# Kernel tuning notes

Hardware: AMD Instinct MI355X
Metric: run time of the kernel (lower is better)

Reference implementation:

```python
import jax, jax.numpy as jnp
import numpy as np

T = 4
THRESH = 1.0
TAU = 1.0
GAMA = 0.5

# Heaviside spike with Gaussian surrogate gradient (SgNormal)
@jax.custom_vjp
def sg_normal(x):
    return (x > 0).astype(x.dtype)

def _sg_fwd(x):
    return (x > 0).astype(x.dtype), x

def _sg_bwd(x, g):
    inv_norm = 1.0 / (GAMA * np.sqrt(2.0 * np.pi).astype(np.float32))
    return (g * jnp.exp(-(x * x) / (2.0 * GAMA * GAMA)) * inv_norm,)

sg_normal.defvjp(_sg_fwd, _sg_bwd)


def setup_inputs() -> dict:
    key = jax.random.key(0)
    x = jax.random.normal(key, (T, 64, 128, 32, 32), dtype=jnp.float32)
    return {"x": x}


def reference(x):
    # LIF recurrence over T timesteps: mem = mem*tau + x[t]; spike = H(mem - thresh); mem = (1-spike)*mem
    def step(mem, xt):
        mem = mem * TAU + xt
        spike = sg_normal(mem - THRESH)
        mem = (1.0 - spike) * mem
        return mem, spike

    mem0 = jnp.zeros(x.shape[1:], dtype=x.dtype)
    _, spikes = jax.lax.scan(step, mem0, x)  # spikes: [T, B, C, H, W]
    return spikes
```

## Files before the change

### kernel.cpp

```cpp
#include <hip/hip_runtime.h>


#define LIF_T 4
#define CHUNKS 4

typedef float f32x4 __attribute__((ext_vector_type(4)));

__device__ __forceinline__ f32x4 lif_step(f32x4& mem, f32x4 xt) {
    mem.x += xt.x;
    mem.y += xt.y;
    mem.z += xt.z;
    mem.w += xt.w;
    f32x4 sp;
    sp.x = (mem.x > 1.0f) ? 1.0f : 0.0f;
    sp.y = (mem.y > 1.0f) ? 1.0f : 0.0f;
    sp.z = (mem.z > 1.0f) ? 1.0f : 0.0f;
    sp.w = (mem.w > 1.0f) ? 1.0f : 0.0f;
    mem.x = (sp.x > 0.f) ? 0.f : mem.x;
    mem.y = (sp.y > 0.f) ? 0.f : mem.y;
    mem.z = (sp.z > 0.f) ? 0.f : mem.z;
    mem.w = (sp.w > 0.f) ? 0.f : mem.w;
    return sp;
}

__global__ __launch_bounds__(256) void
lif_spike_kernel(const float* __restrict__ x, float* __restrict__ out, int n_vec) {
    const int base = blockIdx.x * (256 * CHUNKS) + threadIdx.x;
    const f32x4* __restrict__ xv = reinterpret_cast<const f32x4*>(x);
    f32x4* __restrict__ ov = reinterpret_cast<f32x4*>(out);

    if (base + (CHUNKS - 1) * 256 < n_vec) {
        f32x4 mem[CHUNKS];
#pragma unroll
        for (int c = 0; c < CHUNKS; ++c) mem[c] = (f32x4){0.f, 0.f, 0.f, 0.f};

#pragma unroll
        for (int t = 0; t < LIF_T; ++t) {
            const size_t p = (size_t)t * n_vec + base;
            f32x4 xt[CHUNKS];
#pragma unroll
            for (int c = 0; c < CHUNKS; ++c) xt[c] = xv[p + c * 256];
#pragma unroll
            for (int c = 0; c < CHUNKS; ++c) {
                f32x4 sp = lif_step(mem[c], xt[c]);
                __builtin_nontemporal_store(sp, &ov[p + c * 256]);
            }
        }
    } else {
        f32x4 memc[CHUNKS];
#pragma unroll
        for (int c = 0; c < CHUNKS; ++c) memc[c] = (f32x4){0.f, 0.f, 0.f, 0.f};
#pragma unroll
        for (int t = 0; t < LIF_T; ++t) {
#pragma unroll
            for (int c = 0; c < CHUNKS; ++c) {
                int idx = base + c * 256;
                if (idx < n_vec) {
                    f32x4 sp = lif_step(memc[c], xv[(size_t)t * n_vec + idx]);
                    __builtin_nontemporal_store(sp, &ov[(size_t)t * n_vec + idx]);
                }
            }
        }
    }
}

extern "C" void kernel_launch(void* const* d_in, const int* in_sizes, int n_in,
                              void* d_out, int out_size, void* d_ws, size_t ws_size,
                              hipStream_t stream) {
    const float* x = (const float*)d_in[0];
    float* out = (float*)d_out;

    int n = out_size / LIF_T;
    int n_vec = n / 4;

    const int block = 256;
    int grid = (n_vec + block * CHUNKS - 1) / (block * CHUNKS);
    lif_spike_kernel<<<grid, block, 0, stream>>>(x, out, n_vec);
}
```

Baseline: 227.3 us.

## Stage LIF inputs through LDS with async global_load_lds and smaller per-block chunks

Every thread now issues all four timesteps' loads up front as direct global-to-LDS transfers (`global_load_lds`, 16 bytes per lane). It then waits on vmcnt before each timestep and reads its inputs from LDS. The aim is to have more memory requests in flight per thread before any compute starts, which should hide latency on this bandwidth-bound kernel. Per-block work drops from 1024 to 512 float4 per timestep, which doubles the grid. The trade-offs are LDS allocation, manual waitcnt accounting that stores also affect, and reliance on 16-byte LDS DMA support.

```diff
diff --git a/kernel.cpp b/kernel.cpp
--- a/kernel.cpp
+++ b/kernel.cpp
@@ -2,9 +2,12 @@
 
 
 #define LIF_T 4
-#define CHUNKS 4
+#define CHUNK_F4 512
 
 typedef float f32x4 __attribute__((ext_vector_type(4)));
+
+#define AS1 __attribute__((address_space(1)))
+#define AS3 __attribute__((address_space(3)))
 
 __device__ __forceinline__ f32x4 lif_step(f32x4& mem, f32x4 xt) {
     mem.x += xt.x;
@@ -25,36 +28,53 @@
 
 __global__ __launch_bounds__(256) void
 lif_spike_kernel(const float* __restrict__ x, float* __restrict__ out, int n_vec) {
-    const int base = blockIdx.x * (256 * CHUNKS) + threadIdx.x;
+    __shared__ f32x4 lds[LIF_T][CHUNK_F4];
+
+    const int tid  = threadIdx.x;
+    const int wave = tid >> 6;
+    const int lane = tid & 63;
+    const int b0   = blockIdx.x * CHUNK_F4;
+
     const f32x4* __restrict__ xv = reinterpret_cast<const f32x4*>(x);
     f32x4* __restrict__ ov = reinterpret_cast<f32x4*>(out);
 
-    if (base + (CHUNKS - 1) * 256 < n_vec) {
-        f32x4 mem[CHUNKS];
+    if (b0 + CHUNK_F4 <= n_vec) {
 #pragma unroll
-        for (int c = 0; c < CHUNKS; ++c) mem[c] = (f32x4){0.f, 0.f, 0.f, 0.f};
+        for (int t = 0; t < LIF_T; ++t) {
+#pragma unroll
+            for (int s = 0; s < 2; ++s) {
+                const int l4 = wave * 128 + s * 64;
+                const f32x4* g = xv + (size_t)t * n_vec + b0 + l4 + lane;
+                __builtin_amdgcn_global_load_lds(
+                    (const AS1 void*)g, (AS3 void*)&lds[t][l4], 16, 0, 0);
+            }
+        }
+
+        f32x4 mem[2];
+        mem[0] = (f32x4){0.f, 0.f, 0.f, 0.f};
+        mem[1] = (f32x4){0.f, 0.f, 0.f, 0.f};
 
 #pragma unroll
         for (int t = 0; t < LIF_T; ++t) {
-            const size_t p = (size_t)t * n_vec + base;
-            f32x4 xt[CHUNKS];
+            asm volatile("s_waitcnt vmcnt(6)" ::: "memory");
+            __builtin_amdgcn_sched_barrier(0);
 #pragma unroll
-            for (int c = 0; c < CHUNKS; ++c) xt[c] = xv[p + c * 256];
-#pragma unroll
-            for (int c = 0; c < CHUNKS; ++c) {
-                f32x4 sp = lif_step(mem[c], xt[c]);
-                __builtin_nontemporal_store(sp, &ov[p + c * 256]);
+            for (int c = 0; c < 2; ++c) {
+                const int l4 = wave * 128 + c * 64 + lane;
+                f32x4 xt = lds[t][l4];
+                f32x4 sp = lif_step(mem[c], xt);
+                __builtin_nontemporal_store(sp, &ov[(size_t)t * n_vec + b0 + l4]);
             }
         }
     } else {
-        f32x4 memc[CHUNKS];
-#pragma unroll
-        for (int c = 0; c < CHUNKS; ++c) memc[c] = (f32x4){0.f, 0.f, 0.f, 0.f};
+        f32x4 memc[2];
+        memc[0] = (f32x4){0.f, 0.f, 0.f, 0.f};
+        memc[1] = (f32x4){0.f, 0.f, 0.f, 0.f};
 #pragma unroll
         for (int t = 0; t < LIF_T; ++t) {
 #pragma unroll
-            for (int c = 0; c < CHUNKS; ++c) {
-                int idx = base + c * 256;
+            for (int c = 0; c < 2; ++c) {
+                const int idx = b0 + wave * 128 + c * 64 + lane;
                 if (idx < n_vec) {
                     f32x4 sp = lif_step(memc[c], xv[(size_t)t * n_vec + idx]);
                     __builtin_nontemporal_store(sp, &ov[(size_t)t * n_vec + idx]);
@@ -74,6 +94,6 @@
     int n_vec = n / 4;
 
     const int block = 256;
-    int grid = (n_vec + block * CHUNKS - 1) / (block * CHUNKS);
+    int grid = (n_vec + CHUNK_F4 - 1) / CHUNK_F4;
     lif_spike_kernel<<<grid, block, 0, stream>>>(x, out, n_vec);
 }
```

Measured after the change: 229.4 us. No clear change (+0.9%).
